# Optimization experiments

Hardware: AMD Instinct MI355X
Metric: run time of the kernel (lower is better)

Reference implementation:

```python
import jax, jax.numpy as jnp
import numpy as np

ANCHOR_NUM = 8
CLASS_NUM = 2
IN_DIM = 1024

def setup_inputs() -> dict:
    key = jax.random.key(0)
    k1, k2, k3, k4 = jax.random.split(key, 4)
    batch_input = jax.random.normal(k1, (64, 512, IN_DIM), dtype=jnp.float32)
    # labels in {-1, 0, 1}: -1 = padding, 0 = negative anchor, 1 = positive anchor
    anchor_labels = jax.random.randint(k2, (64, 512, ANCHOR_NUM), 0, 3, dtype=jnp.int64 if jax.config.read('jax_enable_x64') else jnp.int32) - 1
    lim = 1.0 / np.sqrt(IN_DIM)
    W = jax.random.uniform(k3, (IN_DIM, ANCHOR_NUM * CLASS_NUM), dtype=jnp.float32, minval=-lim, maxval=lim)
    b = jax.random.uniform(k4, (ANCHOR_NUM * CLASS_NUM,), dtype=jnp.float32, minval=-lim, maxval=lim)
    return {"batch_input": batch_input, "W": W, "b": b, "anchor_labels": anchor_labels}

def reference(batch_input, W, b, anchor_labels):
    B, S, _ = batch_input.shape
    # logits: (B, S, anchor_num, class_num)
    logits = (jnp.einsum('bsd,dk->bsk', batch_input, W) + b).reshape(B, S, ANCHOR_NUM, CLASS_NUM)
    predict_label = jnp.argmax(logits, axis=3)  # (B, S, A)
    valid = (anchor_labels != -1)
    labels = jnp.maximum(anchor_labels, 0)  # safe class index for padded entries
    logp = jax.nn.log_softmax(logits, axis=-1)
    nll = -jnp.take_along_axis(logp, labels[..., None].astype(jnp.int32), axis=-1)[..., 0]
    # CrossEntropyLoss (mean) over all non-padding anchors == eval-path gather + CE
    vf = valid.astype(logits.dtype)
    loss = jnp.sum(nll * vf) / jnp.maximum(jnp.sum(vf), 1.0)
    # candidate mask stands in for candidate_idx (positive predictions, non-padding)
    candidate_mask = (predict_label == 1) & valid
    return loss, predict_label, candidate_mask
```

## Files before the change

### kernel.cpp

```cpp
#include <hip/hip_runtime.h>
#include <math.h>


#define ROWS   32
#define NW     4
#define KSLICE 256
#define CHUNK  32
#define XSTR   36

__global__ __launch_bounds__(256, 4)
void rpn_main(const float* __restrict__ x, const float* __restrict__ W,
              const float* __restrict__ b, const int* __restrict__ lab,
              float* __restrict__ out, float* __restrict__ ws)
{
    __shared__ float xs[NW * ROWS * XSTR];
    __shared__ float wch[NW * CHUNK * 16];
    float* red = xs;

    const int tid  = threadIdx.x;
    const int wave = tid >> 6;
    const int lane = tid & 63;
    const int r    = lane & 31;
    const int h    = lane >> 5;
    const int row0 = blockIdx.x * ROWS;

    float* xslab = xs + wave * (ROWS * XSTR);
    const float* gx = x + (size_t)row0 * 1024 + wave * KSLICE;

    float acc[8];
#pragma unroll
    for (int c = 0; c < 8; ++c) acc[c] = 0.f;

    for (int ch = 0; ch < KSLICE / CHUNK; ++ch) {
        const float* gsrc = gx + ch * CHUNK;
#pragma unroll
        for (int j = 0; j < 4; ++j) {
            int fl = j * 64 + lane;
            int rr = fl >> 3;
            int c4 = fl & 7;
            float4 v = *(const float4*)(gsrc + (size_t)rr * 1024 + c4 * 4);
            *(float4*)(xslab + rr * XSTR + c4 * 4) = v;
        }
#pragma unroll
        for (int j = 0; j < 2; ++j) {
            int e = (tid + 256 * j) * 4;
            float4 wv = *(const float4*)(W + e + (e >> 9) * 3584 + ch * 512);
            *(float4*)(wch + e) = wv;
        }
        __syncthreads();

        const float* xrow = xslab + r * XSTR;
        const float* wp   = wch + wave * (CHUNK * 16) + h * 8;
#pragma unroll
        for (int t4 = 0; t4 < 8; ++t4) {
            float4 xq = *(const float4*)(xrow + t4 * 4);
#pragma unroll
            for (int i = 0; i < 4; ++i) {
                int dd = t4 * 4 + i;
                float xv = (&xq.x)[i];
                float4 w0 = *(const float4*)(wp + dd * 16);
                float4 w1 = *(const float4*)(wp + dd * 16 + 4);
                acc[0] = fmaf(xv, w0.x, acc[0]);
                acc[1] = fmaf(xv, w0.y, acc[1]);
                acc[2] = fmaf(xv, w0.z, acc[2]);
                acc[3] = fmaf(xv, w0.w, acc[3]);
                acc[4] = fmaf(xv, w1.x, acc[4]);
                acc[5] = fmaf(xv, w1.y, acc[5]);
                acc[6] = fmaf(xv, w1.z, acc[6]);
                acc[7] = fmaf(xv, w1.w, acc[7]);
            }
        }
        __syncthreads();
    }

    {
        float* rp = red + r * 68 + wave * 16 + h * 8;
        *(float4*)(rp)     = make_float4(acc[0], acc[1], acc[2], acc[3]);
        *(float4*)(rp + 4) = make_float4(acc[4], acc[5], acc[6], acc[7]);
    }
    __syncthreads();

    if (tid < ROWS) {
        const int row = row0 + tid;
        float L[16];
#pragma unroll
        for (int c = 0; c < 16; ++c)
            L[c] = red[tid * 68 + c] + red[tid * 68 + 16 + c]
                 + red[tid * 68 + 32 + c] + red[tid * 68 + 48 + c] + b[c];

        const int* labp  = lab + (size_t)row * 8;
        float*     predp = out + 1 + (size_t)row * 8;
        float*     maskp = out + 1 + 262144 + (size_t)row * 8;

        float lsum = 0.f, lcnt = 0.f;
#pragma unroll
        for (int a = 0; a < 8; ++a) {
            float l0 = L[2 * a], l1 = L[2 * a + 1];
            int   lb = labp[a];
            int   pred  = (l1 > l0) ? 1 : 0;
            int   valid = (lb != -1);
            float m   = fmaxf(l0, l1);
            float lse = m + logf(expf(l0 - m) + expf(l1 - m));
            float nll = lse - ((lb == 1) ? l1 : l0);
            if (valid) { lsum += nll; lcnt += 1.f; }
            predp[a] = (float)pred;
            maskp[a] = (pred && valid) ? 1.f : 0.f;
        }

#pragma unroll
        for (int off = 16; off > 0; off >>= 1) {
            lsum += __shfl_down(lsum, off, 32);
            lcnt += __shfl_down(lcnt, off, 32);
        }
        if (tid == 0) {
            atomicAdd(&ws[0], lsum);
            atomicAdd(&ws[1], lcnt);
        }
    }
}

__global__ void rpn_final(const float* __restrict__ ws, float* __restrict__ out)
{
    out[0] = ws[0] / fmaxf(ws[1], 1.f);
}

extern "C" void kernel_launch(void* const* d_in, const int* in_sizes, int n_in,
                              void* d_out, int out_size, void* d_ws, size_t ws_size,
                              hipStream_t stream)
{
    const float* x   = (const float*)d_in[0];
    const float* W   = (const float*)d_in[1];
    const float* b   = (const float*)d_in[2];
    const int*   lab = (const int*)d_in[3];
    float* out = (float*)d_out;
    float* ws  = (float*)d_ws;

    hipMemsetAsync(ws, 0, 2 * sizeof(float), stream);
    rpn_main<<<dim3(1024), dim3(256), 0, stream>>>(x, W, b, lab, out, ws);
    rpn_final<<<dim3(1), dim3(1), 0, stream>>>(ws, out);
}
```

Baseline: 216.7 us.

## Register-prefetch x chunks, read W via scalar loads, widen blocks to 64 rows

The kernel is restructured so each block handles 64 rows with 8 waves, each wave owning a 128-wide K slice. Each lane computes all 16 outputs for one row, with W read directly from global memory through wave-uniform addresses so it can use scalar loads instead of an LDS staging copy. The next x chunk is prefetched into registers while the current one is computed, and the per-chunk __syncthreads are removed because each wave only touches its own LDS slab. The cost is higher register pressure (16 accumulators plus 8 float4 prefetch registers) and half as many blocks.

```diff
diff --git a/kernel.cpp b/kernel.cpp
--- a/kernel.cpp
+++ b/kernel.cpp
@@ -2,81 +2,79 @@
 #include <math.h>
 
 
-#define ROWS   32
-#define NW     4
-#define KSLICE 256
+#define ROWS   64
+#define NW     8
+#define KSLICE 128
 #define CHUNK  32
+#define NCH    (KSLICE/CHUNK)
 #define XSTR   36
+#define RSTR   136
 
-__global__ __launch_bounds__(256, 4)
+__global__ __launch_bounds__(512, 4)
 void rpn_main(const float* __restrict__ x, const float* __restrict__ W,
               const float* __restrict__ b, const int* __restrict__ lab,
               float* __restrict__ out, float* __restrict__ ws)
 {
     __shared__ float xs[NW * ROWS * XSTR];
-    __shared__ float wch[NW * CHUNK * 16];
     float* red = xs;
 
     const int tid  = threadIdx.x;
-    const int wave = tid >> 6;
     const int lane = tid & 63;
-    const int r    = lane & 31;
-    const int h    = lane >> 5;
+    const int ks   = __builtin_amdgcn_readfirstlane(tid >> 6);
     const int row0 = blockIdx.x * ROWS;
 
-    float* xslab = xs + wave * (ROWS * XSTR);
-    const float* gx = x + (size_t)row0 * 1024 + wave * KSLICE;
+    float* slab = xs + ks * (ROWS * XSTR);
+    const float* gbase = x + (size_t)row0 * 1024 + ks * KSLICE;
 
-    float acc[8];
+    float acc[16];
 #pragma unroll
-    for (int c = 0; c < 8; ++c) acc[c] = 0.f;
+    for (int c = 0; c < 16; ++c) acc[c] = 0.f;
 
-    for (int ch = 0; ch < KSLICE / CHUNK; ++ch) {
-        const float* gsrc = gx + ch * CHUNK;
+    float4 pf[8];
 #pragma unroll
-        for (int j = 0; j < 4; ++j) {
+    for (int j = 0; j < 8; ++j) {
+        int fl = j * 64 + lane;
+        pf[j] = *(const float4*)(gbase + (size_t)(fl >> 3) * 1024 + (fl & 7) * 4);
+    }
+
+#pragma unroll 1
+    for (int ch = 0; ch < NCH; ++ch) {
+#pragma unroll
+        for (int j = 0; j < 8; ++j) {
             int fl = j * 64 + lane;
-            int rr = fl >> 3;
-            int c4 = fl & 7;
-            float4 v = *(const float4*)(gsrc + (size_t)rr * 1024 + c4 * 4);
-            *(float4*)(xslab + rr * XSTR + c4 * 4) = v;
+            *(float4*)(slab + (fl >> 3) * XSTR + (fl & 7) * 4) = pf[j];
         }
+        if (ch + 1 < NCH) {
+            const float* g = gbase + (ch + 1) * CHUNK;
 #pragma unroll
-        for (int j = 0; j < 2; ++j) {
-            int e = (tid + 256 * j) * 4;
-            float4 wv = *(const float4*)(W + e + (e >> 9) * 3584 + ch * 512);
-            *(float4*)(wch + e) = wv;
+            for (int j = 0; j < 8; ++j) {
+                int fl = j * 64 + lane;
+                pf[j] = *(const float4*)(g + (size_t)(fl >> 3) * 1024 + (fl & 7) * 4);
+            }
         }
-        __syncthreads();
-
-        const float* xrow = xslab + r * XSTR;
-        const float* wp   = wch + wave * (CHUNK * 16) + h * 8;
+        const float* xrow = slab + lane * XSTR;
+        const float* wk   = W + (size_t)(ks * KSLICE + ch * CHUNK) * 16;
 #pragma unroll
         for (int t4 = 0; t4 < 8; ++t4) {
             float4 xq = *(const float4*)(xrow + t4 * 4);
 #pragma unroll
             for (int i = 0; i < 4; ++i) {
-                int dd = t4 * 4 + i;
                 float xv = (&xq.x)[i];
-                float4 w0 = *(const float4*)(wp + dd * 16);
-                float4 w1 = *(const float4*)(wp + dd * 16 + 4);
-                acc[0] = fmaf(xv, w0.x, acc[0]);
-                acc[1] = fmaf(xv, w0.y, acc[1]);
-                acc[2] = fmaf(xv, w0.z, acc[2]);
-                acc[3] = fmaf(xv, w0.w, acc[3]);
-                acc[4] = fmaf(xv, w1.x, acc[4]);
-                acc[5] = fmaf(xv, w1.y, acc[5]);
-                acc[6] = fmaf(xv, w1.z, acc[6]);
-                acc[7] = fmaf(xv, w1.w, acc[7]);
+                const float* wr = wk + (t4 * 4 + i) * 16;
+#pragma unroll
+                for (int c = 0; c < 16; ++c)
+                    acc[c] = fmaf(xv, wr[c], acc[c]);
             }
         }
-        __syncthreads();
     }
 
+    __syncthreads();
     {
-        float* rp = red + r * 68 + wave * 16 + h * 8;
-        *(float4*)(rp)     = make_float4(acc[0], acc[1], acc[2], acc[3]);
-        *(float4*)(rp + 4) = make_float4(acc[4], acc[5], acc[6], acc[7]);
+        float* rp = red + lane * RSTR + ks * 16;
+        *(float4*)(rp + 0)  = make_float4(acc[0],  acc[1],  acc[2],  acc[3]);
+        *(float4*)(rp + 4)  = make_float4(acc[4],  acc[5],  acc[6],  acc[7]);
+        *(float4*)(rp + 8)  = make_float4(acc[8],  acc[9],  acc[10], acc[11]);
+        *(float4*)(rp + 12) = make_float4(acc[12], acc[13], acc[14], acc[15]);
     }
     __syncthreads();
 
@@ -84,9 +82,12 @@
         const int row = row0 + tid;
         float L[16];
 #pragma unroll
-        for (int c = 0; c < 16; ++c)
-            L[c] = red[tid * 68 + c] + red[tid * 68 + 16 + c]
-                 + red[tid * 68 + 32 + c] + red[tid * 68 + 48 + c] + b[c];
+        for (int c = 0; c < 16; ++c) {
+            float s = 0.f;
+#pragma unroll
+            for (int k = 0; k < NW; ++k) s += red[tid * RSTR + k * 16 + c];
+            L[c] = s + b[c];
+        }
 
         const int* labp  = lab + (size_t)row * 8;
         float*     predp = out + 1 + (size_t)row * 8;
@@ -108,9 +109,9 @@
         }
 
 #pragma unroll
-        for (int off = 16; off > 0; off >>= 1) {
-            lsum += __shfl_down(lsum, off, 32);
-            lcnt += __shfl_down(lcnt, off, 32);
+        for (int off = 32; off > 0; off >>= 1) {
+            lsum += __shfl_down(lsum, off, 64);
+            lcnt += __shfl_down(lcnt, off, 64);
         }
         if (tid == 0) {
             atomicAdd(&ws[0], lsum);
@@ -136,6 +137,6 @@
     float* ws  = (float*)d_ws;
 
     hipMemsetAsync(ws, 0, 2 * sizeof(float), stream);
-    rpn_main<<<dim3(1024), dim3(256), 0, stream>>>(x, W, b, lab, out, ws);
+    rpn_main<<<dim3(512), dim3(512), 0, stream>>>(x, W, b, lab, out, ws);
     rpn_final<<<dim3(1), dim3(1), 0, stream>>>(ws, out);
 }
```

New measurement: 237.9 us. 1.1x slower.
